# Optimization experiments

Measured on AMD Instinct MI355X. Metric: run time of the kernel, lower is better.

The kernel has to match this reference:

```python
import jax, jax.numpy as jnp
import numpy as np

THETA = 0.5  # forward default arg
ALPHA = 0.2  # LeakyReLU negative slope
NEG_INF = -9e15


def setup_inputs() -> dict:
    key = jax.random.key(0)
    k1, k2, k3, k4, k5 = jax.random.split(key, 5)
    N, F_IN, F_OUT = 8192, 256, 256
    h = jax.random.normal(k1, (N, F_IN), dtype=jnp.float32)
    adj = jax.random.randint(k2, (N, N), 0, 2, dtype=jnp.int32)
    cv_values = jax.random.uniform(k3, (N,), dtype=jnp.float32)
    # xavier_uniform with gain=1.414
    g = 1.414
    bw = g * np.sqrt(6.0 / (F_IN + F_OUT))
    W = jax.random.uniform(k4, (F_IN, F_OUT), dtype=jnp.float32, minval=-bw, maxval=bw)
    ba = g * np.sqrt(6.0 / (2 * F_OUT + 1))
    a = jax.random.uniform(k5, (2 * F_OUT, 1), dtype=jnp.float32, minval=-ba, maxval=ba)
    return {"h": h, "adj": adj, "cv_values": cv_values, "W": W, "a": a}


def reference(h, adj, cv_values, W, a):
    # Wh: [N, F_out]
    Wh = h @ W
    F_out = Wh.shape[1]
    a1 = a[:F_out, 0]   # [F_out]
    a2 = a[F_out:, 0]   # [F_out]
    # e_ij = LeakyReLU([Wh_i ; Wh_j] . a) = LeakyReLU(Wh_i.a1 + Wh_j.a2)
    f1 = Wh @ a1        # [N]
    f2 = Wh @ a2        # [N]
    e = jax.nn.leaky_relu(f1[:, None] + f2[None, :], negative_slope=ALPHA)
    # CV bias: theta * cv_i broadcast across row i
    e = e + THETA * cv_values[:, None]
    att = jnp.where(adj > 0, e, jnp.float32(NEG_INF))
    att = jax.nn.softmax(att, axis=1)
    # dropout is identity in eval mode (training=False)
    h_prime = att @ Wh  # [N, F_out]
    return jax.nn.elu(h_prime)  # concat=True branch
```

## Files before the change

### kernel.cpp

```cpp
#include <hip/hip_runtime.h>
#include <cstdint>
#include <cstddef>

typedef _Float16 half8 __attribute__((ext_vector_type(8)));
typedef _Float16 half4 __attribute__((ext_vector_type(4)));
typedef float f32x4 __attribute__((ext_vector_type(4)));

#define GAT_N 8192
#define GAT_F 256
#define GAT_NQ 8
#define GAT_ALPHA 0.2f
#define GAT_LOG2E 1.4426950408889634f

__device__ inline unsigned enc_f32(float x) {
    unsigned b = __float_as_uint(x);
    return (b & 0x80000000u) ? ~b : (b | 0x80000000u);
}
__device__ inline float dec_f32(unsigned u) {
    unsigned b = (u & 0x80000000u) ? (u ^ 0x80000000u) : ~u;
    return __uint_as_float(b);
}

__device__ inline unsigned pack8(int4 v0, int4 v1) {
    return (unsigned)(v0.x > 0)        | ((unsigned)(v0.y > 0) << 1)
         | ((unsigned)(v0.z > 0) << 2) | ((unsigned)(v0.w > 0) << 3)
         | ((unsigned)(v1.x > 0) << 4) | ((unsigned)(v1.y > 0) << 5)
         | ((unsigned)(v1.z > 0) << 6) | ((unsigned)(v1.w > 0) << 7);
}


__global__ __launch_bounds__(256) void gat_k0b_convert(
    const float* __restrict__ W, _Float16* __restrict__ WT,
    unsigned* __restrict__ f2mxEnc)
{
    const int g = blockIdx.x * 256 + threadIdx.x;
    if (g == 0) *f2mxEnc = 0u;
    const int k = g >> 8, n = g & 255;
    WT[n * GAT_F + k] = (_Float16)W[g];
}

__global__ __launch_bounds__(256, 2) void gat_k1_gemm(
    const float* __restrict__ h, const _Float16* __restrict__ WT,
    const float* __restrict__ a, _Float16* __restrict__ whT2,
    float* __restrict__ f1L, float* __restrict__ f2L,
    unsigned* __restrict__ f2mxEnc)
{
    __shared__ float sP1[4][16], sP2[4][16];
    const int wv = threadIdx.x >> 6;
    const int lane = threadIdx.x & 63;
    const int l15 = lane & 15;
    const int quad = lane >> 4;
    const int r0 = blockIdx.x * 16;

    f32x4 acc[4];
    #pragma unroll
    for (int t = 0; t < 4; ++t) { f32x4 z = {0.f,0.f,0.f,0.f}; acc[t] = z; }

    #pragma unroll
    for (int k0 = 0; k0 < GAT_F; k0 += 32) {
        const float* ap = h + (size_t)(r0 + l15) * GAT_F + k0 + quad * 8;
        const float4 a0 = *reinterpret_cast<const float4*>(ap);
        const float4 a1 = *reinterpret_cast<const float4*>(ap + 4);
        half8 af;
        af[0] = (_Float16)a0.x; af[1] = (_Float16)a0.y;
        af[2] = (_Float16)a0.z; af[3] = (_Float16)a0.w;
        af[4] = (_Float16)a1.x; af[5] = (_Float16)a1.y;
        af[6] = (_Float16)a1.z; af[7] = (_Float16)a1.w;
        #pragma unroll
        for (int t = 0; t < 4; ++t) {
            half8 bf = *reinterpret_cast<const half8*>(
                WT + (size_t)(wv * 64 + t * 16 + l15) * GAT_F + k0 + quad * 8);
            acc[t] = __builtin_amdgcn_mfma_f32_16x16x32_f16(af, bf, acc[t], 0, 0, 0);
        }
    }

    float p1[4] = {0.f,0.f,0.f,0.f}, p2[4] = {0.f,0.f,0.f,0.f};
    #pragma unroll
    for (int t = 0; t < 4; ++t) {
        float a1c = a[wv * 64 + t * 16 + l15];
        float a2c = a[GAT_F + wv * 64 + t * 16 + l15];
        #pragma unroll
        for (int r = 0; r < 4; ++r) {
            p1[r] = fmaf(acc[t][r], a1c, p1[r]);
            p2[r] = fmaf(acc[t][r], a2c, p2[r]);
        }
    }
    #pragma unroll
    for (int off = 1; off < 16; off <<= 1) {
        #pragma unroll
        for (int r = 0; r < 4; ++r) {
            p1[r] += __shfl_xor(p1[r], off);
            p2[r] += __shfl_xor(p2[r], off);
        }
    }
    if (l15 == 0) {
        #pragma unroll
        for (int r = 0; r < 4; ++r) {
            sP1[wv][quad * 4 + r] = p1[r];
            sP2[wv][quad * 4 + r] = p2[r];
        }
    }
    __syncthreads();
    if (threadIdx.x < 16) {
        const int row = threadIdx.x;
        const float s1 = (sP1[0][row] + sP1[1][row] + sP1[2][row] + sP1[3][row]) * GAT_LOG2E;
        const float s2 = (sP2[0][row] + sP2[1][row] + sP2[2][row] + sP2[3][row]) * GAT_LOG2E;
        f1L[r0 + row] = s1;
        f2L[r0 + row] = s2;
        float mx = s2;
        #pragma unroll
        for (int off = 1; off < 16; off <<= 1) mx = fmaxf(mx, __shfl_xor(mx, off));
        if (row == 0) atomicMax(f2mxEnc, enc_f32(mx));
    }

    const size_t tbase = (size_t)(r0 >> 6) * 16384
                       + (((r0 & 63) >> 3) + (quad >> 1)) * 2048
                       + (quad & 1) * 4;
    #pragma unroll
    for (int t = 0; t < 4; ++t) {
        const int c = wv * 64 + t * 16 + l15;
        half4 hv;
        #pragma unroll
        for (int r = 0; r < 4; ++r) hv[r] = (_Float16)acc[t][r];
        *reinterpret_cast<half4*>(whT2 + tbase + c * 8) = hv;
    }
}

__global__ __launch_bounds__(256, 2) void gat_k3_attn(
    const int* __restrict__ adj, const float* __restrict__ f1L,
    const float* __restrict__ f2L, const unsigned* __restrict__ f2mxEnc,
    const _Float16* __restrict__ whT2,
    _Float16* __restrict__ Ph,
    float* __restrict__ L)
{
    __shared__ __align__(16) _Float16 sB[2][16384];

    const int bx = blockIdx.x;
    const int q  = bx & 7;
    const int rb = bx >> 3;
    const int wv = threadIdx.x >> 6;
    const int lane = threadIdx.x & 63;
    const int l15 = lane & 15;
    const int quad = lane >> 4;

    const int kq = q * 1024;
    const int r0 = rb * 128 + wv * 32;
    const int rA = r0 + l15;
    const int rB = rA + 16;

    const float fmxL = dec_f32(*f2mxEnc);
    const float f1A = f1L[rA];
    const float f1B = f1L[rB];
    const float sA = f1A + fmxL;
    const float sBv = f1B + fmxL;
    const float CA = fmaxf(sA, GAT_ALPHA * sA);
    const float CB = fmaxf(sBv, GAT_ALPHA * sBv);
    const float uA = f1A - CA, vA = GAT_ALPHA * f1A - CA;
    const float uB = f1B - CB, vB = GAT_ALPHA * f1B - CB;

    f32x4 acc[2][16];
    #pragma unroll
    for (int s = 0; s < 2; ++s)
        #pragma unroll
        for (int t = 0; t < 16; ++t) {
            f32x4 z = {0.f,0.f,0.f,0.f};
            acc[s][t] = z;
        }
    float d0 = 0.f, d1 = 0.f;

    const int* aprA = adj + (size_t)rA * GAT_N + kq + quad * 8;
    const int* aprB = adj + (size_t)rB * GAT_N + kq + quad * 8;
    const float* f2q = f2L + kq + quad * 8;

    int4 xA0, xA1, xA2, xA3, xB0, xB1, xB2, xB3;
    #define ADJLOAD(s)                                                         \
        {                                                                      \
            const int* pa = aprA + (s) * 64;                                   \
            const int* pb = aprB + (s) * 64;                                   \
            xA0 = *reinterpret_cast<const int4*>(pa);                          \
            xA1 = *reinterpret_cast<const int4*>(pa + 4);                      \
            xA2 = *reinterpret_cast<const int4*>(pa + 32);                     \
            xA3 = *reinterpret_cast<const int4*>(pa + 36);                     \
            xB0 = *reinterpret_cast<const int4*>(pb);                          \
            xB1 = *reinterpret_cast<const int4*>(pb + 4);                      \
            xB2 = *reinterpret_cast<const int4*>(pb + 32);                     \
            xB3 = *reinterpret_cast<const int4*>(pb + 36);                     \
        }
    #define ADJPACK(ma, mb)                                                    \
        {                                                                      \
            ma = pack8(xA0, xA1) | (pack8(xA2, xA3) << 8);                     \
            mb = pack8(xB0, xB1) | (pack8(xB2, xB3) << 8);                     \
        }

    const _Float16* tile0 = whT2 + (size_t)(q * 16) * 16384 + (size_t)lane * 8;
    #define STAGE(buf, step)                                                   \
        {                                                                      \
            _Pragma("unroll")                                                  \
            for (int i = 0; i < 8; ++i) {                                      \
                const int off = wv * 4096 + i * 512;                           \
                const _Float16* gp = tile0 + (size_t)(step) * 16384 + off;     \
                _Float16* lp = &sB[buf][off];                                  \
                __builtin_amdgcn_global_load_lds(                              \
                    (const __attribute__((address_space(1))) void*)gp,         \
                    (__attribute__((address_space(3))) void*)lp, 16, 0, 0);    \
            }                                                                  \
        }

    ADJLOAD(0)
    float4 nfa = *reinterpret_cast<const float4*>(f2q);
    float4 nfb = *reinterpret_cast<const float4*>(f2q + 4);
    STAGE(0, 0)
    unsigned cmA, cmB;
    ADJPACK(cmA, cmB)
    unsigned nmA = 0, nmB = 0;
    __syncthreads();

    for (int step = 0; step < 16; ++step) {
        const int cur = step & 1;
        if (step < 15) {
            ADJLOAD(step + 1)
            STAGE(1 - cur, step + 1)
        }

        #pragma unroll
        for (int k2 = 0; k2 < 2; ++k2) {
            const int u = step * 2 + k2;
            const float4 cfa = nfa, cfb = nfb;
            if (u < 31) {
                nfa = *reinterpret_cast<const float4*>(f2q + (u + 1) * 32);
                nfb = *reinterpret_cast<const float4*>(f2q + (u + 1) * 32 + 4);
            }
            const unsigned mA = (cmA >> (k2 * 8)) & 0xffu;
            const unsigned mB = (cmB >> (k2 * 8)) & 0xffu;
            const float f2v[8] = {cfa.x, cfa.y, cfa.z, cfa.w,
                                  cfb.x, cfb.y, cfb.z, cfb.w};
            float af2[8];
            #pragma unroll
            for (int j = 0; j < 8; ++j) af2[j] = GAT_ALPHA * f2v[j];

            half8 pA, pB;
            #pragma unroll
            for (int j = 0; j < 8; ++j) {
                float pa = __builtin_amdgcn_exp2f(fmaxf(uA + f2v[j], vA + af2[j]));
                pa = (mA & (1u << j)) ? pa : 0.f;
                d0 += pa;
                pA[j] = (_Float16)pa;
                float pb = __builtin_amdgcn_exp2f(fmaxf(uB + f2v[j], vB + af2[j]));
                pb = (mB & (1u << j)) ? pb : 0.f;
                d1 += pb;
                pB[j] = (_Float16)pb;
            }

            const int lbase = (k2 * 4 + quad) * 2048 + l15 * 8;
            #pragma unroll
            for (int t = 0; t < 16; ++t) {
                half8 bf = *reinterpret_cast<const half8*>(
                    &sB[cur][lbase + t * 128]);
                acc[0][t] = __builtin_amdgcn_mfma_f32_16x16x32_f16(pA, bf, acc[0][t], 0, 0, 0);
                acc[1][t] = __builtin_amdgcn_mfma_f32_16x16x32_f16(pB, bf, acc[1][t], 0, 0, 0);
            }
        }
        if (step < 15) ADJPACK(nmA, nmB)
        __syncthreads();
        cmA = nmA; cmB = nmB;
    }
    #undef STAGE
    #undef ADJLOAD
    #undef ADJPACK

    d0 += __shfl_xor(d0, 16); d0 += __shfl_xor(d0, 32);
    d1 += __shfl_xor(d1, 16); d1 += __shfl_xor(d1, 32);
    if (lane < 16) {
        float* Lq = L + q * GAT_N;
        Lq[rA] = d0; Lq[rB] = d1;
    }

    const int wid = rb * 4 + wv;
    _Float16* Pq = Ph + ((size_t)q * 256 + wid) * 8192;
    #pragma unroll
    for (int s = 0; s < 2; ++s)
        #pragma unroll
        for (int t = 0; t < 16; ++t) {
            half4 hv;
            #pragma unroll
            for (int r = 0; r < 4; ++r) hv[r] = (_Float16)acc[s][t][r];
            *reinterpret_cast<half4*>(Pq + (size_t)(((s * 16 + t) * 64 + lane) * 4)) = hv;
        }
}

__global__ __launch_bounds__(256) void gat_k4_final(
    const _Float16* __restrict__ Ph, const float* __restrict__ L,
    float* __restrict__ out)
{
    const int tid = threadIdx.x;
    const int wid = blockIdx.x >> 3;
    __shared__ float s_rl[32];
    if (tid < 32) {
        const int row = wid * 32 + tid;
        float s = 0.f;
        #pragma unroll
        for (int q = 0; q < GAT_NQ; ++q) s += L[q * GAT_N + row];
        s_rl[tid] = 1.0f / fmaxf(s, 1e-30f);
    }
    __syncthreads();

    const int idx = blockIdx.x * 256 + tid;
    const int rem = idx & 2047;
    const int lane = rem & 63;
    const int st = rem >> 6;
    const int s = st >> 4, t = st & 15;
    const int l15 = lane & 15, quad = lane >> 4;
    const int lrow0 = s * 16 + quad * 4;
    const int col = t * 16 + l15;

    float accv[4] = {0.f, 0.f, 0.f, 0.f};
    #pragma unroll
    for (int q = 0; q < GAT_NQ; ++q) {
        half4 v = *reinterpret_cast<const half4*>(
            Ph + ((size_t)q * 256 + wid) * 8192 + (size_t)rem * 4);
        #pragma unroll
        for (int r = 0; r < 4; ++r) accv[r] += (float)v[r];
    }
    #pragma unroll
    for (int r = 0; r < 4; ++r) {
        const float v = accv[r] * s_rl[lrow0 + r];
        const float o = v > 0.f ? v : expm1f(v);
        out[(size_t)(wid * 32 + lrow0 + r) * GAT_F + col] = o;
    }
}

extern "C" void kernel_launch(void* const* d_in, const int* in_sizes, int n_in,
                              void* d_out, int out_size, void* d_ws, size_t ws_size,
                              hipStream_t stream)
{
    const float* h   = (const float*)d_in[0];
    const int*   adj = (const int*)d_in[1];
    const float* W   = (const float*)d_in[3];
    const float* a   = (const float*)d_in[4];
    float* out = (float*)d_out;
    char* ws = (char*)d_ws;

    const size_t SLAB = (size_t)GAT_N * GAT_F * 2;

    size_t off = 0;
    _Float16* whT2 = (_Float16*)(ws + off); off += SLAB;
    _Float16* Ph  = (_Float16*)(ws + off); off += GAT_NQ * SLAB;
    _Float16* WT  = (_Float16*)(ws + off); off += (size_t)GAT_F * GAT_F * 2;
    float* f1L = (float*)(ws + off); off += GAT_N * 4;
    float* f2L = (float*)(ws + off); off += GAT_N * 4;
    float* L   = (float*)(ws + off); off += GAT_NQ * GAT_N * 4;
    unsigned* f2mxEnc = (unsigned*)(ws + off); off += 256;

    gat_k0b_convert<<<256, 256, 0, stream>>>(W, WT, f2mxEnc);
    gat_k1_gemm<<<512, 256, 0, stream>>>(h, WT, a, whT2, f1L, f2L, f2mxEnc);
    gat_k3_attn<<<512, 256, 0, stream>>>(adj, f1L, f2L, f2mxEnc, whT2, Ph, L);
    gat_k4_final<<<2048, 256, 0, stream>>>(Ph, L, out);
}
```

Before: 430.1 us.

## Read Wh B-operand directly from global memory and use nontemporal loads/stores

The attention kernel no longer stages Wh tiles into double-buffered LDS with global_load_lds and barriers. Each lane now reads its B fragments straight from global memory, counting on L2/L1 to serve the reuse across waves. The adjacency stream, the partial-output stores and the final kernel's loads and stores now use nontemporal hints to keep them from polluting the cache. This removes the LDS traffic and per-step barriers, but each wave now issues redundant global loads that sit on the MFMA critical path with no software prefetch.

```diff
diff --git a/kernel.cpp b/kernel.cpp
--- a/kernel.cpp
+++ b/kernel.cpp
@@ -5,6 +5,7 @@
 typedef _Float16 half8 __attribute__((ext_vector_type(8)));
 typedef _Float16 half4 __attribute__((ext_vector_type(4)));
 typedef float f32x4 __attribute__((ext_vector_type(4)));
+typedef int iv4 __attribute__((ext_vector_type(4)));
 
 #define GAT_N 8192
 #define GAT_F 256
@@ -21,11 +22,11 @@
     return __uint_as_float(b);
 }
 
-__device__ inline unsigned pack8(int4 v0, int4 v1) {
-    return (unsigned)(v0.x > 0)        | ((unsigned)(v0.y > 0) << 1)
-         | ((unsigned)(v0.z > 0) << 2) | ((unsigned)(v0.w > 0) << 3)
-         | ((unsigned)(v1.x > 0) << 4) | ((unsigned)(v1.y > 0) << 5)
-         | ((unsigned)(v1.z > 0) << 6) | ((unsigned)(v1.w > 0) << 7);
+__device__ inline unsigned pack8(iv4 v0, iv4 v1) {
+    return (unsigned)(v0[0] > 0)        | ((unsigned)(v0[1] > 0) << 1)
+         | ((unsigned)(v0[2] > 0) << 2) | ((unsigned)(v0[3] > 0) << 3)
+         | ((unsigned)(v1[0] > 0) << 4) | ((unsigned)(v1[1] > 0) << 5)
+         | ((unsigned)(v1[2] > 0) << 6) | ((unsigned)(v1[3] > 0) << 7);
 }
 
 
@@ -133,8 +134,6 @@
     _Float16* __restrict__ Ph,
     float* __restrict__ L)
 {
-    __shared__ __align__(16) _Float16 sB[2][16384];
-
     const int bx = blockIdx.x;
     const int q  = bx & 7;
     const int rb = bx >> 3;
@@ -172,19 +171,22 @@
     const int* aprB = adj + (size_t)rB * GAT_N + kq + quad * 8;
     const float* f2q = f2L + kq + quad * 8;
 
-    int4 xA0, xA1, xA2, xA3, xB0, xB1, xB2, xB3;
+    const _Float16* bfp0 = whT2 + (size_t)(q * 16) * 16384
+                         + (size_t)quad * 2048 + (size_t)l15 * 8;
+
+    iv4 xA0, xA1, xA2, xA3, xB0, xB1, xB2, xB3;
     #define ADJLOAD(s)                                                         \
         {                                                                      \
-            const int* pa = aprA + (s) * 64;                                   \
-            const int* pb = aprB + (s) * 64;                                   \
-            xA0 = *reinterpret_cast<const int4*>(pa);                          \
-            xA1 = *reinterpret_cast<const int4*>(pa + 4);                      \
-            xA2 = *reinterpret_cast<const int4*>(pa + 32);                     \
-            xA3 = *reinterpret_cast<const int4*>(pa + 36);                     \
-            xB0 = *reinterpret_cast<const int4*>(pb);                          \
-            xB1 = *reinterpret_cast<const int4*>(pb + 4);                      \
-            xB2 = *reinterpret_cast<const int4*>(pb + 32);                     \
-            xB3 = *reinterpret_cast<const int4*>(pb + 36);                     \
+            const iv4* pa = reinterpret_cast<const iv4*>(aprA + (s) * 64);     \
+            const iv4* pb = reinterpret_cast<const iv4*>(aprB + (s) * 64);     \
+            xA0 = __builtin_nontemporal_load(pa);                              \
+            xA1 = __builtin_nontemporal_load(pa + 1);                          \
+            xA2 = __builtin_nontemporal_load(pa + 8);                          \
+            xA3 = __builtin_nontemporal_load(pa + 9);                          \
+            xB0 = __builtin_nontemporal_load(pb);                              \
+            xB1 = __builtin_nontemporal_load(pb + 1);                          \
+            xB2 = __builtin_nontemporal_load(pb + 8);                          \
+            xB3 = __builtin_nontemporal_load(pb + 9);                          \
         }
     #define ADJPACK(ma, mb)                                                    \
         {                                                                      \
@@ -192,35 +194,16 @@
             mb = pack8(xB0, xB1) | (pack8(xB2, xB3) << 8);                     \
         }
 
-    const _Float16* tile0 = whT2 + (size_t)(q * 16) * 16384 + (size_t)lane * 8;
-    #define STAGE(buf, step)                                                   \
-        {                                                                      \
-            _Pragma("unroll")                                                  \
-            for (int i = 0; i < 8; ++i) {                                      \
-                const int off = wv * 4096 + i * 512;                           \
-                const _Float16* gp = tile0 + (size_t)(step) * 16384 + off;     \
-                _Float16* lp = &sB[buf][off];                                  \
-                __builtin_amdgcn_global_load_lds(                              \
-                    (const __attribute__((address_space(1))) void*)gp,         \
-                    (__attribute__((address_space(3))) void*)lp, 16, 0, 0);    \
-            }                                                                  \
-        }
-
     ADJLOAD(0)
     float4 nfa = *reinterpret_cast<const float4*>(f2q);
     float4 nfb = *reinterpret_cast<const float4*>(f2q + 4);
-    STAGE(0, 0)
     unsigned cmA, cmB;
     ADJPACK(cmA, cmB)
     unsigned nmA = 0, nmB = 0;
-    __syncthreads();
 
     for (int step = 0; step < 16; ++step) {
-        const int cur = step & 1;
-        if (step < 15) {
-            ADJLOAD(step + 1)
-            STAGE(1 - cur, step + 1)
-        }
+        if (step < 15) ADJLOAD(step + 1)
+        const _Float16* bstep = bfp0 + (size_t)step * 16384;
 
         #pragma unroll
         for (int k2 = 0; k2 < 2; ++k2) {
@@ -251,20 +234,17 @@
                 pB[j] = (_Float16)pb;
             }
 
-            const int lbase = (k2 * 4 + quad) * 2048 + l15 * 8;
+            const _Float16* bk = bstep + k2 * 8192;
             #pragma unroll
             for (int t = 0; t < 16; ++t) {
-                half8 bf = *reinterpret_cast<const half8*>(
-                    &sB[cur][lbase + t * 128]);
+                half8 bf = *reinterpret_cast<const half8*>(bk + t * 128);
                 acc[0][t] = __builtin_amdgcn_mfma_f32_16x16x32_f16(pA, bf, acc[0][t], 0, 0, 0);
                 acc[1][t] = __builtin_amdgcn_mfma_f32_16x16x32_f16(pB, bf, acc[1][t], 0, 0, 0);
             }
         }
         if (step < 15) ADJPACK(nmA, nmB)
-        __syncthreads();
         cmA = nmA; cmB = nmB;
     }
-    #undef STAGE
     #undef ADJLOAD
     #undef ADJPACK
 
@@ -284,7 +264,8 @@
             half4 hv;
             #pragma unroll
             for (int r = 0; r < 4; ++r) hv[r] = (_Float16)acc[s][t][r];
-            *reinterpret_cast<half4*>(Pq + (size_t)(((s * 16 + t) * 64 + lane) * 4)) = hv;
+            __builtin_nontemporal_store(hv,
+                reinterpret_cast<half4*>(Pq + (size_t)(((s * 16 + t) * 64 + lane) * 4)));
         }
 }
 
@@ -316,8 +297,8 @@
     float accv[4] = {0.f, 0.f, 0.f, 0.f};
     #pragma unroll
     for (int q = 0; q < GAT_NQ; ++q) {
-        half4 v = *reinterpret_cast<const half4*>(
-            Ph + ((size_t)q * 256 + wid) * 8192 + (size_t)rem * 4);
+        half4 v = __builtin_nontemporal_load(reinterpret_cast<const half4*>(
+            Ph + ((size_t)q * 256 + wid) * 8192 + (size_t)rem * 4));
         #pragma unroll
         for (int r = 0; r < 4; ++r) accv[r] += (float)v[r];
     }
@@ -325,7 +306,8 @@
     for (int r = 0; r < 4; ++r) {
         const float v = accv[r] * s_rl[lrow0 + r];
         const float o = v > 0.f ? v : expm1f(v);
-        out[(size_t)(wid * 32 + lrow0 + r) * GAT_F + col] = o;
+        __builtin_nontemporal_store(o,
+            &out[(size_t)(wid * 32 + lrow0 + r) * GAT_F + col]);
     }
 }
 
```

New measurement: 470.5 us. 1.09x slower.

## Deepen adjacency prefetch to two steps and stage f2 in LDS

Applied to the files above, without the earlier changes.

The attention kernel now double-buffers adjacency loads two steps ahead in alternating register sets. It replaces the full __syncthreads with a partial vmcnt wait plus s_barrier, so the next whT tile and adjacency loads can stay in flight across the barrier. The f2 row slice is loaded once into shared memory instead of being prefetched per sub-step from global memory. This costs extra registers for the second adjacency set and depends on hand-counted vmcnt ordering, which could be fragile or hurt occupancy.

```diff
diff --git a/kernel.cpp b/kernel.cpp
--- a/kernel.cpp
+++ b/kernel.cpp
@@ -5,6 +5,7 @@
 typedef _Float16 half8 __attribute__((ext_vector_type(8)));
 typedef _Float16 half4 __attribute__((ext_vector_type(4)));
 typedef float f32x4 __attribute__((ext_vector_type(4)));
+typedef int iv4 __attribute__((ext_vector_type(4)));
 
 #define GAT_N 8192
 #define GAT_F 256
@@ -21,11 +22,11 @@
     return __uint_as_float(b);
 }
 
-__device__ inline unsigned pack8(int4 v0, int4 v1) {
-    return (unsigned)(v0.x > 0)        | ((unsigned)(v0.y > 0) << 1)
-         | ((unsigned)(v0.z > 0) << 2) | ((unsigned)(v0.w > 0) << 3)
-         | ((unsigned)(v1.x > 0) << 4) | ((unsigned)(v1.y > 0) << 5)
-         | ((unsigned)(v1.z > 0) << 6) | ((unsigned)(v1.w > 0) << 7);
+__device__ inline unsigned pack8(iv4 v0, iv4 v1) {
+    return (unsigned)(v0[0] > 0)        | ((unsigned)(v0[1] > 0) << 1)
+         | ((unsigned)(v0[2] > 0) << 2) | ((unsigned)(v0[3] > 0) << 3)
+         | ((unsigned)(v1[0] > 0) << 4) | ((unsigned)(v1[1] > 0) << 5)
+         | ((unsigned)(v1[2] > 0) << 6) | ((unsigned)(v1[3] > 0) << 7);
 }
 
 
@@ -134,6 +135,7 @@
     float* __restrict__ L)
 {
     __shared__ __align__(16) _Float16 sB[2][16384];
+    __shared__ __align__(16) float sF2[1024];
 
     const int bx = blockIdx.x;
     const int q  = bx & 7;
@@ -158,6 +160,11 @@
     const float uA = f1A - CA, vA = GAT_ALPHA * f1A - CA;
     const float uB = f1B - CB, vB = GAT_ALPHA * f1B - CB;
 
+    {
+        const float4 v = *reinterpret_cast<const float4*>(f2L + kq + threadIdx.x * 4);
+        *reinterpret_cast<float4*>(&sF2[threadIdx.x * 4]) = v;
+    }
+
     f32x4 acc[2][16];
     #pragma unroll
     for (int s = 0; s < 2; ++s)
@@ -170,26 +177,26 @@
 
     const int* aprA = adj + (size_t)rA * GAT_N + kq + quad * 8;
     const int* aprB = adj + (size_t)rB * GAT_N + kq + quad * 8;
-    const float* f2q = f2L + kq + quad * 8;
-
-    int4 xA0, xA1, xA2, xA3, xB0, xB1, xB2, xB3;
-    #define ADJLOAD(s)                                                         \
+
+    iv4 p0a0, p0a1, p0a2, p0a3, p0b0, p0b1, p0b2, p0b3;
+    iv4 p1a0, p1a1, p1a2, p1a3, p1b0, p1b1, p1b2, p1b3;
+    #define ADJLOAD(SET, s)                                                    \
         {                                                                      \
             const int* pa = aprA + (s) * 64;                                   \
             const int* pb = aprB + (s) * 64;                                   \
-            xA0 = *reinterpret_cast<const int4*>(pa);                          \
-            xA1 = *reinterpret_cast<const int4*>(pa + 4);                      \
-            xA2 = *reinterpret_cast<const int4*>(pa + 32);                     \
-            xA3 = *reinterpret_cast<const int4*>(pa + 36);                     \
-            xB0 = *reinterpret_cast<const int4*>(pb);                          \
-            xB1 = *reinterpret_cast<const int4*>(pb + 4);                      \
-            xB2 = *reinterpret_cast<const int4*>(pb + 32);                     \
-            xB3 = *reinterpret_cast<const int4*>(pb + 36);                     \
-        }
-    #define ADJPACK(ma, mb)                                                    \
+            SET##a0 = *reinterpret_cast<const iv4*>(pa);                       \
+            SET##a1 = *reinterpret_cast<const iv4*>(pa + 4);                   \
+            SET##a2 = *reinterpret_cast<const iv4*>(pa + 32);                  \
+            SET##a3 = *reinterpret_cast<const iv4*>(pa + 36);                  \
+            SET##b0 = *reinterpret_cast<const iv4*>(pb);                       \
+            SET##b1 = *reinterpret_cast<const iv4*>(pb + 4);                   \
+            SET##b2 = *reinterpret_cast<const iv4*>(pb + 32);                  \
+            SET##b3 = *reinterpret_cast<const iv4*>(pb + 36);                  \
+        }
+    #define ADJPACK(SET, ma, mb)                                               \
         {                                                                      \
-            ma = pack8(xA0, xA1) | (pack8(xA2, xA3) << 8);                     \
-            mb = pack8(xB0, xB1) | (pack8(xB2, xB3) << 8);                     \
+            ma = pack8(SET##a0, SET##a1) | (pack8(SET##a2, SET##a3) << 8);     \
+            mb = pack8(SET##b0, SET##b1) | (pack8(SET##b2, SET##b3) << 8);     \
         }
 
     const _Float16* tile0 = whT2 + (size_t)(q * 16) * 16384 + (size_t)lane * 8;
@@ -206,30 +213,14 @@
             }                                                                  \
         }
 
-    ADJLOAD(0)
-    float4 nfa = *reinterpret_cast<const float4*>(f2q);
-    float4 nfb = *reinterpret_cast<const float4*>(f2q + 4);
-    STAGE(0, 0)
-    unsigned cmA, cmB;
-    ADJPACK(cmA, cmB)
-    unsigned nmA = 0, nmB = 0;
-    __syncthreads();
-
-    for (int step = 0; step < 16; ++step) {
-        const int cur = step & 1;
-        if (step < 15) {
-            ADJLOAD(step + 1)
-            STAGE(1 - cur, step + 1)
-        }
-
+    unsigned cmA, cmB, nmA = 0, nmB = 0;
+
+    auto step_body = [&](int cur, int step) {
         #pragma unroll
         for (int k2 = 0; k2 < 2; ++k2) {
-            const int u = step * 2 + k2;
-            const float4 cfa = nfa, cfb = nfb;
-            if (u < 31) {
-                nfa = *reinterpret_cast<const float4*>(f2q + (u + 1) * 32);
-                nfb = *reinterpret_cast<const float4*>(f2q + (u + 1) * 32 + 4);
-            }
+            const float* fp = &sF2[step * 64 + k2 * 32 + quad * 8];
+            const float4 cfa = *reinterpret_cast<const float4*>(fp);
+            const float4 cfb = *reinterpret_cast<const float4*>(fp + 4);
             const unsigned mA = (cmA >> (k2 * 8)) & 0xffu;
             const unsigned mB = (cmB >> (k2 * 8)) & 0xffu;
             const float f2v[8] = {cfa.x, cfa.y, cfa.z, cfa.w,
@@ -260,10 +251,36 @@
                 acc[1][t] = __builtin_amdgcn_mfma_f32_16x16x32_f16(pB, bf, acc[1][t], 0, 0, 0);
             }
         }
-        if (step < 15) ADJPACK(nmA, nmB)
-        __syncthreads();
+    };
+
+    STAGE(0, 0)
+    ADJLOAD(p0, 0)
+    ADJPACK(p0, cmA, cmB)
+    __syncthreads();
+    ADJLOAD(p1, 1)
+
+    for (int step = 0; step < 15; ++step) {
+        const int cur = step & 1;
+        asm volatile("s_waitcnt vmcnt(8)" ::: "memory");
+        __builtin_amdgcn_sched_barrier(0);
+        __builtin_amdgcn_s_barrier();
+        STAGE(1 - cur, step + 1)
+        if (step < 14) {
+            if (cur == 0) ADJLOAD(p0, step + 2)
+            else          ADJLOAD(p1, step + 2)
+        }
+
+        step_body(cur, step);
+
+        if (cur == 0) ADJPACK(p1, nmA, nmB)
+        else          ADJPACK(p0, nmA, nmB)
         cmA = nmA; cmB = nmB;
     }
+    asm volatile("s_waitcnt vmcnt(0)" ::: "memory");
+    __builtin_amdgcn_sched_barrier(0);
+    __builtin_amdgcn_s_barrier();
+    step_body(1, 15);
+
     #undef STAGE
     #undef ADJLOAD
     #undef ADJPACK
```

After: 483.4 us. 1.12x slower.
